# Optimization experiments

Measured on AMD Instinct MI355X. Metric: run time of the kernel, lower is better.

The kernel has to match this reference:

```python
import jax, jax.numpy as jnp
import numpy as np

NEG_SLOPE = 0.2  # PyG GATConv default leaky_relu slope
EPS = 1e-16


def setup_inputs() -> dict:
    key = jax.random.key(0)
    ks = jax.random.split(key, 6)
    N, F, H, C, E = 50000, 128, 8, 16, 600000
    node_features = jax.random.normal(ks[0], (N, F), dtype=jnp.float32)
    edge_index = jax.random.randint(ks[1], (2, E), 0, N, dtype=jnp.int64)
    W = jax.random.normal(ks[2], (F, H * C), dtype=jnp.float32) * (1.0 / np.sqrt(F))
    att_src = jax.random.normal(ks[3], (H, C), dtype=jnp.float32)
    att_dst = jax.random.normal(ks[4], (H, C), dtype=jnp.float32)
    bias = jnp.zeros((H * C,), dtype=jnp.float32)
    return {"node_features": node_features, "edge_index": edge_index,
            "W": W, "att_src": att_src, "att_dst": att_dst, "bias": bias}


def reference(node_features, edge_index, W, att_src, att_dst, bias):
    N = node_features.shape[0]
    H, C = att_src.shape
    # Linear transform, split into heads: [N, H, C]
    x = (node_features @ W).reshape(N, H, C)
    # add self loops (PyG default add_self_loops=True)
    loop = jnp.arange(N, dtype=edge_index.dtype)
    src = jnp.concatenate([edge_index[0], loop])  # message source j
    dst = jnp.concatenate([edge_index[1], loop])  # message target i
    # per-node attention logits [N, H]
    a_src = jnp.einsum('nhc,hc->nh', x, att_src)
    a_dst = jnp.einsum('nhc,hc->nh', x, att_dst)
    # edge-wise logits with leaky relu [E, H]
    alpha = jax.nn.leaky_relu(a_src[src] + a_dst[dst], NEG_SLOPE)
    # softmax over incoming edges of each target node (segment softmax)
    amax = jax.ops.segment_max(alpha, dst, num_segments=N)
    alpha = jnp.exp(alpha - amax[dst])
    asum = jax.ops.segment_sum(alpha, dst, num_segments=N)
    alpha = alpha / (asum[dst] + EPS)
    # weighted scatter-aggregate of source features [N, H, C]
    msgs = x[src] * alpha[:, :, None]
    out = jax.ops.segment_sum(msgs, dst, num_segments=N)
    out = out.reshape(N, H * C) + bias
    # SELU activation; dropout is identity in eval mode
    return jax.nn.selu(out)
```

## Files before the change

kernel.cpp:

```cpp
#include <hip/hip_runtime.h>
#include <hip/hip_fp16.h>

#define LEAKY_SLOPE 0.2f

typedef _Float16 h8 __attribute__((ext_vector_type(8)));
typedef float f32x4 __attribute__((ext_vector_type(4)));

__device__ __forceinline__ float leaky_relu_f(float v) { return v > 0.f ? v : LEAKY_SLOPE * v; }
__device__ __forceinline__ float selu_f(float v) {
    const float sc = 1.0507009873554805f, al = 1.6732632423543772f;
    return v > 0.f ? sc * v : sc * al * expm1f(v);
}

__device__ __forceinline__ int detect_is64_wave(const int* __restrict__ e32) {
    int v = e32[2 * (threadIdx.x & 63) + 1];
    unsigned long long b = __ballot(v != 0);
    return b == 0ull ? 1 : 0;
}

__device__ __forceinline__ int edge_at(const void* edges, long long idx, int is64) {
    return is64 ? (int)((const long long*)edges)[idx] : ((const int*)edges)[idx];
}

__global__ void prep_kernel(int* __restrict__ deg, int n,
                            const float* __restrict__ W, _Float16* __restrict__ Wt) {
    int i = blockIdx.x * blockDim.x + threadIdx.x;
    if (i < n) deg[i] = 0;
    if (i < 128 * 128) {
        int k = i >> 7, c = i & 127;
        Wt[c * 128 + k] = (_Float16)W[i];
    }
}

__global__ __launch_bounds__(256) void gemm_kernel(const float* __restrict__ feats,
                                                   const _Float16* __restrict__ Wt,
                                                   const float* __restrict__ att_src,
                                                   const float* __restrict__ att_dst,
                                                   __half* __restrict__ xh,
                                                   float* __restrict__ a_src,
                                                   float* __restrict__ a_dst, int N) {
    __shared__ __align__(16) _Float16 Af[64][136];
    __shared__ __align__(16) _Float16 Bt[128][136];
    const int t = threadIdx.x;

    if (blockIdx.x == 0) {
        if (t < 64) *(__half2*)&xh[(long long)N * 128 + 2 * t] = __floats2half2_rn(0.f, 0.f);
        if (t < 8) a_src[N * 8 + t] = -1e30f;
    }

    {
        const float4* F4 = (const float4*)feats;
#pragma unroll
        for (int i = 0; i < 8; i++) {
            int q = t + i * 256;
            int row = q >> 5;
            int c = (q & 31) * 4;
            int r_abs = blockIdx.x * 64 + row;
            if (r_abs >= N) r_abs = N - 1;
            float4 v = F4[(long long)r_abs * 32 + (q & 31)];
            union { _Float16 h[4]; uint2 u; } tmp;
            tmp.h[0] = (_Float16)v.x; tmp.h[1] = (_Float16)v.y;
            tmp.h[2] = (_Float16)v.z; tmp.h[3] = (_Float16)v.w;
            *(uint2*)&Af[row][c] = tmp.u;
        }
    }
    {
        const uint4* Wt4 = (const uint4*)Wt;
#pragma unroll
        for (int i = 0; i < 8; i++) {
            int q = t + i * 256;
            int c = q >> 4;
            int k0 = (q & 15) * 8;
            *(uint4*)&Bt[c][k0] = Wt4[q];
        }
    }
    __syncthreads();

    const int l = t & 63;
    const int w = t >> 6;
    const int lr = l & 15;
    const int lg = l >> 4;

    f32x4 acc[8];
#pragma unroll
    for (int n = 0; n < 8; n++) acc[n] = (f32x4){0.f, 0.f, 0.f, 0.f};

#pragma unroll
    for (int kk = 0; kk < 4; kk++) {
        const int k0 = kk * 32 + lg * 8;
        h8 a = *(const h8*)&Af[16 * w + lr][k0];
#pragma unroll
        for (int n = 0; n < 8; n++) {
            h8 b = *(const h8*)&Bt[16 * n + lr][k0];
            acc[n] = __builtin_amdgcn_mfma_f32_16x16x32_f16(a, b, acc[n], 0, 0, 0);
        }
    }

    const int rbase = blockIdx.x * 64 + 16 * w + lg * 4;
#pragma unroll
    for (int n = 0; n < 8; n++) {
        float asv = att_src[n * 16 + lr];
        float adv = att_dst[n * 16 + lr];
#pragma unroll
        for (int r = 0; r < 4; r++) {
            int row_abs = rbase + r;
            float v = acc[n][r];
            if (row_abs < N) xh[(long long)row_abs * 128 + 16 * n + lr] = (__half)v;
            float ps = v * asv;
            float pd = v * adv;
            ps += __shfl_xor(ps, 1); ps += __shfl_xor(ps, 2);
            ps += __shfl_xor(ps, 4); ps += __shfl_xor(ps, 8);
            pd += __shfl_xor(pd, 1); pd += __shfl_xor(pd, 2);
            pd += __shfl_xor(pd, 4); pd += __shfl_xor(pd, 8);
            if (lr == n && row_abs < N) {
                a_src[row_abs * 8 + n] = ps;
                a_dst[row_abs * 8 + n] = pd;
            }
        }
    }
}

__global__ void hist_kernel(const void* __restrict__ edges, long long E,
                            int* __restrict__ deg, int* __restrict__ rank) {
    int is64 = detect_is64_wave((const int*)edges);
    long long stride = (long long)gridDim.x * blockDim.x;
    for (long long e = (long long)blockIdx.x * blockDim.x + threadIdx.x; e < E; e += stride) {
        int dst = edge_at(edges, E + e, is64);
        rank[e] = atomicAdd(&deg[dst], 1);
    }
}

__global__ __launch_bounds__(256) void scan1_kernel(const int* __restrict__ deg,
                                                    int* __restrict__ offs,
                                                    int* __restrict__ bsum, int N) {
    __shared__ int lds[256];
    int t = threadIdx.x;
    int base = blockIdx.x * 1024 + t * 4;
    int v[4];
    int s = 0;
#pragma unroll
    for (int i = 0; i < 4; i++) {
        v[i] = (base + i < N) ? ((deg[base + i] + 7) & ~7) : 0;
        s += v[i];
    }
    lds[t] = s;
    __syncthreads();
    for (int off = 1; off < 256; off <<= 1) {
        int u = (t >= off) ? lds[t - off] : 0;
        __syncthreads();
        lds[t] += u;
        __syncthreads();
    }
    if (t == 255) bsum[blockIdx.x] = lds[255];
    int run = (t == 0) ? 0 : lds[t - 1];
#pragma unroll
    for (int i = 0; i < 4; i++) {
        if (base + i < N) offs[base + i] = run;
        run += v[i];
    }
}

__global__ __launch_bounds__(1024) void scan2_kernel(int* __restrict__ bsum, int nb) {
    __shared__ int lds[1024];
    int t = threadIdx.x;
    int v = (t < nb) ? bsum[t] : 0;
    lds[t] = v;
    __syncthreads();
    for (int off = 1; off < 1024; off <<= 1) {
        int u = (t >= off) ? lds[t - off] : 0;
        __syncthreads();
        lds[t] += u;
        __syncthreads();
    }
    if (t < nb) bsum[t] = lds[t] - v;
    if (t == nb - 1) bsum[nb] = lds[t];
}

__global__ void scan3_kernel(int* __restrict__ offs, const int* __restrict__ bsum,
                             const int* __restrict__ deg, int* __restrict__ csr,
                             int N, int nb) {
    int idx = blockIdx.x * blockDim.x + threadIdx.x;
    if (idx < N) {
        int o = offs[idx] + bsum[idx >> 10];
        offs[idx] = o;
        int d = deg[idx];
        int pd = (d + 7) & ~7;
        for (int q = o + d; q < o + pd; q++) csr[q] = N;
    }
    if (idx == N) offs[N] = bsum[nb];
}

__global__ void scatter_kernel(const void* __restrict__ edges, long long E,
                               const int* __restrict__ offs, const int* __restrict__ rank,
                               int* __restrict__ csr) {
    int is64 = detect_is64_wave((const int*)edges);
    long long stride = (long long)gridDim.x * blockDim.x;
    for (long long e = (long long)blockIdx.x * blockDim.x + threadIdx.x; e < E; e += stride) {
        int src = edge_at(edges, e, is64);
        int dst = edge_at(edges, E + e, is64);
        csr[offs[dst] + rank[e]] = src;
    }
}

__global__ __launch_bounds__(256) void agg_kernel(const __half* __restrict__ xh,
                                                  const float* __restrict__ a_src,
                                                  const float* __restrict__ a_dst,
                                                  const int* __restrict__ offs,
                                                  const int* __restrict__ csr,
                                                  const float* __restrict__ bias,
                                                  float* __restrict__ out, int N) {
    int node = blockIdx.x * 4 + (threadIdx.x >> 6);
    if (node >= N) return;
    int l = threadIdx.x & 63;
    int h8i = l & 7;
    int e8 = l >> 3;
    int hg = l >> 3;

    float ad_w = a_dst[node * 8 + h8i];
    float wself = expf(leaky_relu_f(a_src[node * 8 + h8i] + ad_w));
    float spart = (e8 == 0) ? wself : 0.f;

    float wself_h = __shfl(wself, hg);
    float2 xs = __half22float2(*(const __half2*)&xh[(long long)node * 128 + 2 * l]);
    float accx = wself_h * xs.x;
    float accy = wself_h * xs.y;

    int beg = offs[node], end = offs[node + 1];
    int srcv = 0;
    float w = 0.f;
    if (beg < end) {
        srcv = csr[beg + e8];
        w = expf(leaky_relu_f(a_src[srcv * 8 + h8i] + ad_w));
    }
    for (int p = beg; p < end; p += 8) {
        spart += w;
        int pn = p + 8;
        int srcv_n = 0;
        float asv_n = 0.f;
        bool more = pn < end;
        if (more) {
            srcv_n = csr[pn + e8];
            asv_n = a_src[srcv_n * 8 + h8i];
        }
        float wcur = w;
        int srcv_c = srcv;
#pragma unroll
        for (int e = 0; e < 8; e++) {
            int src = __shfl(srcv_c, e * 8);
            float we = __shfl(wcur, e * 8 + hg);
            float2 xv = __half22float2(*(const __half2*)&xh[(long long)src * 128 + 2 * l]);
            accx = fmaf(we, xv.x, accx);
            accy = fmaf(we, xv.y, accy);
        }
        w = more ? expf(leaky_relu_f(asv_n + ad_w)) : 0.f;
        srcv = srcv_n;
    }
    spart += __shfl_xor(spart, 8);
    spart += __shfl_xor(spart, 16);
    spart += __shfl_xor(spart, 32);
    float s = __shfl(spart, hg);
    float inv = 1.f / (s + 1e-16f);

    float2 b = *(const float2*)&bias[2 * l];
    float2 o;
    o.x = selu_f(fmaf(accx, inv, b.x));
    o.y = selu_f(fmaf(accy, inv, b.y));
    *(float2*)&out[(long long)node * 128 + 2 * l] = o;
}

extern "C" void kernel_launch(void* const* d_in, const int* in_sizes, int n_in,
                              void* d_out, int out_size, void* d_ws, size_t ws_size,
                              hipStream_t stream) {
    const float* feats   = (const float*)d_in[0];
    const void*  edges   = d_in[1];
    const float* W       = (const float*)d_in[2];
    const float* att_src = (const float*)d_in[3];
    const float* att_dst = (const float*)d_in[4];
    const float* bias    = (const float*)d_in[5];

    const int N = in_sizes[0] / 128;
    const long long E = in_sizes[1] / 2;
    const long long fillE = E + 7LL * N;
    float* out = (float*)d_out;

    char* ws = (char*)d_ws;
    __half*   xh    = (__half*)ws;   ws += (size_t)(N + 1) * 128 * 2;
    float*    a_src = (float*)ws;    ws += (size_t)(N + 1) * 8 * 4;
    float*    a_dst = (float*)ws;    ws += (size_t)N * 8 * 4;
    _Float16* Wt    = (_Float16*)ws; ws += 128 * 128 * 2;
    int*      deg   = (int*)ws;      ws += (size_t)N * 4;
    int*      offs  = (int*)ws;      ws += (size_t)(N + 1) * 4;
    int*      rank  = (int*)ws;      ws += (size_t)E * 4;
    int*      bsum  = (int*)ws;      ws += 1028 * 4;
    int*      csr   = (int*)ws;      ws += (size_t)fillE * 4;

    int nb = (N + 1023) / 1024;
    prep_kernel<<<(N + 255) / 256, 256, 0, stream>>>(deg, N, W, Wt);
    hist_kernel<<<2048, 256, 0, stream>>>(edges, E, deg, rank);
    scan1_kernel<<<nb, 256, 0, stream>>>(deg, offs, bsum, N);
    scan2_kernel<<<1, 1024, 0, stream>>>(bsum, nb);
    scan3_kernel<<<(N + 256) / 256, 256, 0, stream>>>(offs, bsum, deg, csr, N, nb);
    gemm_kernel<<<(N + 63) / 64, 256, 0, stream>>>(feats, Wt, att_src, att_dst, xh, a_src, a_dst, N);
    scatter_kernel<<<2048, 256, 0, stream>>>(edges, E, offs, rank, csr);
    agg_kernel<<<(N + 3) / 4, 256, 0, stream>>>(xh, a_src, a_dst, offs, csr, bias, out, N);
}
```

Measured before the change: 114.7 us.

## Fuse histogram into GEMM launch and replace three-pass scan with lookback scan

Runs the degree histogram in extra blocks of the GEMM kernel, so the atomic-heavy edge pass overlaps the feature transform. It also replaces the three-kernel prefix scan with a single-pass decoupled lookback scan that writes offsets and padding in one launch. Together these cut the launch count from eight to five and remove idle gaps between small kernels. The cost is that the lookback spin-wait relies on earlier blocks making progress, and the state array needs zeroing in prep.

```diff
diff --git a/kernel.cpp b/kernel.cpp
--- a/kernel.cpp
+++ b/kernel.cpp
@@ -23,27 +23,41 @@
 }
 
 __global__ void prep_kernel(int* __restrict__ deg, int n,
-                            const float* __restrict__ W, _Float16* __restrict__ Wt) {
+                            const float* __restrict__ W, _Float16* __restrict__ Wt,
+                            int* __restrict__ state, int nstate) {
     int i = blockIdx.x * blockDim.x + threadIdx.x;
     if (i < n) deg[i] = 0;
+    if (i < nstate) state[i] = 0;
     if (i < 128 * 128) {
         int k = i >> 7, c = i & 127;
         Wt[c * 128 + k] = (_Float16)W[i];
     }
 }
 
-__global__ __launch_bounds__(256) void gemm_kernel(const float* __restrict__ feats,
-                                                   const _Float16* __restrict__ Wt,
-                                                   const float* __restrict__ att_src,
-                                                   const float* __restrict__ att_dst,
-                                                   __half* __restrict__ xh,
-                                                   float* __restrict__ a_src,
-                                                   float* __restrict__ a_dst, int N) {
+__global__ __launch_bounds__(256) void gemmhist_kernel(
+    const float* __restrict__ feats, const _Float16* __restrict__ Wt,
+    const float* __restrict__ att_src, const float* __restrict__ att_dst,
+    __half* __restrict__ xh, float* __restrict__ a_src, float* __restrict__ a_dst,
+    int N, int gemmBlocks,
+    const void* __restrict__ edges, long long E,
+    int* __restrict__ deg, int* __restrict__ rank) {
     __shared__ __align__(16) _Float16 Af[64][136];
     __shared__ __align__(16) _Float16 Bt[128][136];
     const int t = threadIdx.x;
 
-    if (blockIdx.x == 0) {
+    if ((int)blockIdx.x >= gemmBlocks) {
+        int is64 = detect_is64_wave((const int*)edges);
+        long long hstride = (long long)(gridDim.x - gemmBlocks) * blockDim.x;
+        for (long long e = (long long)((int)blockIdx.x - gemmBlocks) * blockDim.x + t;
+             e < E; e += hstride) {
+            int dst = edge_at(edges, E + e, is64);
+            rank[e] = atomicAdd(&deg[dst], 1);
+        }
+        return;
+    }
+
+    const int bid = blockIdx.x;
+    if (bid == 0) {
         if (t < 64) *(__half2*)&xh[(long long)N * 128 + 2 * t] = __floats2half2_rn(0.f, 0.f);
         if (t < 8) a_src[N * 8 + t] = -1e30f;
     }
@@ -55,7 +69,7 @@
             int q = t + i * 256;
             int row = q >> 5;
             int c = (q & 31) * 4;
-            int r_abs = blockIdx.x * 64 + row;
+            int r_abs = bid * 64 + row;
             if (r_abs >= N) r_abs = N - 1;
             float4 v = F4[(long long)r_abs * 32 + (q & 31)];
             union { _Float16 h[4]; uint2 u; } tmp;
@@ -96,7 +110,7 @@
         }
     }
 
-    const int rbase = blockIdx.x * 64 + 16 * w + lg * 4;
+    const int rbase = bid * 64 + 16 * w + lg * 4;
 #pragma unroll
     for (int n = 0; n < 8; n++) {
         float asv = att_src[n * 16 + lr];
@@ -120,27 +134,21 @@
     }
 }
 
-__global__ void hist_kernel(const void* __restrict__ edges, long long E,
-                            int* __restrict__ deg, int* __restrict__ rank) {
-    int is64 = detect_is64_wave((const int*)edges);
-    long long stride = (long long)gridDim.x * blockDim.x;
-    for (long long e = (long long)blockIdx.x * blockDim.x + threadIdx.x; e < E; e += stride) {
-        int dst = edge_at(edges, E + e, is64);
-        rank[e] = atomicAdd(&deg[dst], 1);
-    }
-}
-
-__global__ __launch_bounds__(256) void scan1_kernel(const int* __restrict__ deg,
-                                                    int* __restrict__ offs,
-                                                    int* __restrict__ bsum, int N) {
+__global__ __launch_bounds__(256) void scanlb_kernel(const int* __restrict__ deg,
+                                                     int* __restrict__ offs,
+                                                     int* __restrict__ csr,
+                                                     int* __restrict__ state,
+                                                     int N, int nb) {
     __shared__ int lds[256];
-    int t = threadIdx.x;
-    int base = blockIdx.x * 1024 + t * 4;
-    int v[4];
-    int s = 0;
+    __shared__ int s_excl;
+    const int b = blockIdx.x, t = threadIdx.x;
+    const int base = b * 1024 + t * 4;
+
+    int d[4], v[4], s = 0;
 #pragma unroll
     for (int i = 0; i < 4; i++) {
-        v[i] = (base + i < N) ? ((deg[base + i] + 7) & ~7) : 0;
+        d[i] = (base + i < N) ? deg[base + i] : 0;
+        v[i] = (d[i] + 7) & ~7;
         s += v[i];
     }
     lds[t] = s;
@@ -151,43 +159,46 @@
         lds[t] += u;
         __syncthreads();
     }
-    if (t == 255) bsum[blockIdx.x] = lds[255];
-    int run = (t == 0) ? 0 : lds[t - 1];
+    const int total = lds[255];
+    const int local_excl = (t == 0) ? 0 : lds[t - 1];
+
+    if (t == 0) {
+        if (b == 0) {
+            __hip_atomic_store(&state[0], (total << 2) | 2, __ATOMIC_RELEASE,
+                               __HIP_MEMORY_SCOPE_AGENT);
+            s_excl = 0;
+        } else {
+            __hip_atomic_store(&state[b], (total << 2) | 1, __ATOMIC_RELEASE,
+                               __HIP_MEMORY_SCOPE_AGENT);
+            int excl = 0;
+            for (int j = b - 1; j >= 0; j--) {
+                int st;
+                do {
+                    st = __hip_atomic_load(&state[j], __ATOMIC_ACQUIRE,
+                                           __HIP_MEMORY_SCOPE_AGENT);
+                } while ((st & 3) == 0);
+                excl += st >> 2;
+                if ((st & 3) == 2) break;
+            }
+            __hip_atomic_store(&state[b], ((excl + total) << 2) | 2, __ATOMIC_RELEASE,
+                               __HIP_MEMORY_SCOPE_AGENT);
+            s_excl = excl;
+        }
+    }
+    __syncthreads();
+    const int excl = s_excl;
+
+    int run = excl + local_excl;
 #pragma unroll
     for (int i = 0; i < 4; i++) {
-        if (base + i < N) offs[base + i] = run;
+        int idx = base + i;
+        if (idx < N) {
+            offs[idx] = run;
+            for (int q = run + d[i]; q < run + v[i]; q++) csr[q] = N;
+        }
         run += v[i];
     }
-}
-
-__global__ __launch_bounds__(1024) void scan2_kernel(int* __restrict__ bsum, int nb) {
-    __shared__ int lds[1024];
-    int t = threadIdx.x;
-    int v = (t < nb) ? bsum[t] : 0;
-    lds[t] = v;
-    __syncthreads();
-    for (int off = 1; off < 1024; off <<= 1) {
-        int u = (t >= off) ? lds[t - off] : 0;
-        __syncthreads();
-        lds[t] += u;
-        __syncthreads();
-    }
-    if (t < nb) bsum[t] = lds[t] - v;
-    if (t == nb - 1) bsum[nb] = lds[t];
-}
-
-__global__ void scan3_kernel(int* __restrict__ offs, const int* __restrict__ bsum,
-                             const int* __restrict__ deg, int* __restrict__ csr,
-                             int N, int nb) {
-    int idx = blockIdx.x * blockDim.x + threadIdx.x;
-    if (idx < N) {
-        int o = offs[idx] + bsum[idx >> 10];
-        offs[idx] = o;
-        int d = deg[idx];
-        int pd = (d + 7) & ~7;
-        for (int q = o + d; q < o + pd; q++) csr[q] = N;
-    }
-    if (idx == N) offs[N] = bsum[nb];
+    if (b == nb - 1 && t == 255) offs[N] = excl + total;
 }
 
 __global__ void scatter_kernel(const void* __restrict__ edges, long long E,
@@ -291,16 +302,17 @@
     int*      deg   = (int*)ws;      ws += (size_t)N * 4;
     int*      offs  = (int*)ws;      ws += (size_t)(N + 1) * 4;
     int*      rank  = (int*)ws;      ws += (size_t)E * 4;
-    int*      bsum  = (int*)ws;      ws += 1028 * 4;
+    int*      state = (int*)ws;      ws += 64 * 4;
     int*      csr   = (int*)ws;      ws += (size_t)fillE * 4;
 
-    int nb = (N + 1023) / 1024;
-    prep_kernel<<<(N + 255) / 256, 256, 0, stream>>>(deg, N, W, Wt);
-    hist_kernel<<<2048, 256, 0, stream>>>(edges, E, deg, rank);
-    scan1_kernel<<<nb, 256, 0, stream>>>(deg, offs, bsum, N);
-    scan2_kernel<<<1, 1024, 0, stream>>>(bsum, nb);
-    scan3_kernel<<<(N + 256) / 256, 256, 0, stream>>>(offs, bsum, deg, csr, N, nb);
-    gemm_kernel<<<(N + 63) / 64, 256, 0, stream>>>(feats, Wt, att_src, att_dst, xh, a_src, a_dst, N);
+    const int nb = (N + 1023) / 1024;
+    const int gemmBlocks = (N + 63) / 64;
+    const int histBlocks = 1024;
+
+    prep_kernel<<<(N + 255) / 256, 256, 0, stream>>>(deg, N, W, Wt, state, nb + 1);
+    gemmhist_kernel<<<gemmBlocks + histBlocks, 256, 0, stream>>>(
+        feats, Wt, att_src, att_dst, xh, a_src, a_dst, N, gemmBlocks, edges, E, deg, rank);
+    scanlb_kernel<<<nb, 256, 0, stream>>>(deg, offs, csr, state, N, nb);
     scatter_kernel<<<2048, 256, 0, stream>>>(edges, E, offs, rank, csr);
     agg_kernel<<<(N + 3) / 4, 256, 0, stream>>>(xh, a_src, a_dst, offs, csr, bias, out, N);
 }
```

New measurement: 109.7 us. 1.05x faster.
